# Performance work log

Hardware: AMD Instinct MI355X
Metric: run time of the kernel (lower is better)

Reference implementation:

```python
import jax, jax.numpy as jnp
import numpy as np

B, D_IN, M, D_MEM = 65536, 64, 2048, 64


def setup_inputs() -> dict:
    key = jax.random.key(0)
    k = jax.random.split(key, 5)
    glorot = lambda kk, shape: jax.random.uniform(
        kk, shape, jnp.float32,
        -jnp.sqrt(6.0 / (shape[0] + shape[1])), jnp.sqrt(6.0 / (shape[0] + shape[1])))
    return {
        "inputs": jax.random.normal(k[0], (B, D_IN), jnp.float32),
        "W_att": glorot(k[1], (D_IN, M)),
        "b_att": jnp.zeros((M,), jnp.float32),
        "W_write": glorot(k[2], (D_IN, D_MEM)),
        "b_write": jnp.zeros((D_MEM,), jnp.float32),
        "memory": glorot(k[3], (M, D_MEM)),
        "update_gate": jnp.full((M,), 0.5, jnp.float32),
    }


def reference(inputs, W_att, b_att, W_write, b_write, memory, update_gate):
    # Read attention: Dense(memory_size, softmax) -> [B, M]
    read_attention = jax.nn.softmax(inputs @ W_att + b_att, axis=-1)
    # Read: [B, M] @ [M, Dm] -> [B, Dm]
    read_vector = read_attention @ memory
    # Write candidate: Dense(memory_dim, tanh) -> [B, Dm]
    candidate_write = jnp.tanh(inputs @ W_write + b_write)
    aggregated_write = jnp.mean(candidate_write, axis=0)[None, :]  # [1, Dm]
    write_attention = jnp.mean(read_attention, axis=0)             # [M]
    update_weights = (write_attention * update_gate)[:, None]      # [M, 1]
    # Gated in-place memory update (returned as new state)
    new_memory = memory * (1.0 - update_weights) + update_weights * aggregated_write
    return read_vector, new_memory
```

## Files before the change

### kernel.cpp

```cpp
#include <hip/hip_runtime.h>
#include <hip/hip_bf16.h>

typedef unsigned int   u32;
typedef unsigned short u16;

typedef __bf16 bf16x8 __attribute__((ext_vector_type(8)));
typedef float  f32x4  __attribute__((ext_vector_type(4)));
typedef u32    u32x4  __attribute__((ext_vector_type(4)));
typedef u32    u32x2  __attribute__((ext_vector_type(2)));

union Frag { u32x4 u; bf16x8 b; };

#define MFMA16 __builtin_amdgcn_mfma_f32_16x16x32_bf16

#define B_ROWS 65536
#define D_IN   64
#define M_SZ   2048
#define D_MEM  64

#define WT_OFF      0
#define MEMT_OFF    262144
#define WWT_OFF     524288
#define CSF_OFF     532480
#define AGF_OFF     540672
#define CSP_OFF     540928
#define AGP_OFF     8929536
#define WS_REQUIRED 9191680

#define L2E 1.4426950408889634f

__device__ __forceinline__ float bf2f(u16 h) { return __uint_as_float(((u32)h) << 16); }
__device__ __forceinline__ u16 f2bf(float f) {
    u32 u = __float_as_uint(f);
    return (u16)((u + 0x7FFFu + ((u >> 16) & 1u)) >> 16);
}
#if defined(__has_builtin) && __has_builtin(__builtin_amdgcn_exp2f)
__device__ __forceinline__ float exp2fast(float x) { return __builtin_amdgcn_exp2f(x); }
#else
__device__ __forceinline__ float exp2fast(float x) { return __expf(x * 0.6931471805599453f); }
#endif
__device__ __forceinline__ float tanh_fast(float x) {
    const float e = exp2fast(x * (2.0f * L2E));
    return 1.0f - 2.0f * __builtin_amdgcn_rcpf(e + 1.0f);
}
__device__ __forceinline__ bool detect_bf16(const void* ug) {
    return ((const u32*)ug)[0] == 0x3F003F00u;
}
__device__ __forceinline__ float load_elem(const void* p, size_t i, bool isbf) {
    return isbf ? bf2f(((const u16*)p)[i]) : ((const float*)p)[i];
}

__device__ __forceinline__ u32 cvtpk_bf16(float lo, float hi) {
    u32 r;
    asm("v_cvt_pk_bf16_f32 %0, %1, %2" : "=v"(r) : "v"(lo), "v"(hi));
    return r;
}
#if defined(__has_builtin) && __has_builtin(__builtin_amdgcn_permlane32_swap) && \
    __has_builtin(__builtin_amdgcn_permlane16_swap)
__device__ __forceinline__ void pl32swap(u32& a, u32& b) {
    u32x2 r = __builtin_amdgcn_permlane32_swap(a, b, false, false);
    a = r[0]; b = r[1];
}
__device__ __forceinline__ void pl16swap(u32& a, u32& b) {
    u32x2 r = __builtin_amdgcn_permlane16_swap(a, b, false, false);
    a = r[0]; b = r[1];
}
#else
__device__ __forceinline__ void pl32swap(u32& a, u32& b) {
    asm("v_permlane32_swap_b32 %0, %1" : "+v"(a), "+v"(b));
}
__device__ __forceinline__ void pl16swap(u32& a, u32& b) {
    asm("v_permlane16_swap_b32 %0, %1" : "+v"(a), "+v"(b));
}
#endif
template<int CTRL>
__device__ __forceinline__ float xadd(float v) {
    int x = __builtin_amdgcn_update_dpp(0, __float_as_int(v), CTRL, 0xF, 0xF, true);
    return v + __int_as_float(x);
}

__global__ void __launch_bounds__(256)
prep_kernel(const void* Watt, const void* mem_in, const void* Wwr, const void* ug,
            u16* Wt, u16* memT, u16* Wwt, float* CSF)
{
    const bool isbf = detect_bf16(ug);
    const int b = blockIdx.x;
    const int t = threadIdx.x;
    if (b == 65) {
        for (int i = t; i < 2112; i += 256) CSF[i] = 0.f;
        return;
    }
    __shared__ u16 tile[64][65];
    const void* src; u16* dst; int R, C, rb, cb;
    if (b < 32)      { src = Watt;   dst = Wt;   R = 64;   C = 2048; rb = 0;           cb = b * 64; }
    else if (b < 64) { src = mem_in; dst = memT; R = 2048; C = 64;   rb = (b-32) * 64; cb = 0;      }
    else             { src = Wwr;    dst = Wwt;  R = 64;   C = 64;   rb = 0;           cb = 0;      }

#pragma unroll
    for (int j = 0; j < 16; ++j) {
        int e = j * 256 + t;
        int r = e >> 6, c = e & 63;
        float v = load_elem(src, (size_t)(rb + r) * C + cb + c, isbf);
        tile[r][c] = f2bf(v);
    }
    __syncthreads();
#pragma unroll
    for (int j = 0; j < 16; ++j) {
        int e = j * 256 + t;
        int c2 = e >> 6, r2 = e & 63;
        dst[(size_t)(cb + c2) * R + rb + r2] = tile[r2][c2];
    }
}

__global__ void __launch_bounds__(256, 2)
main_kernel(const void* x_in, const void* batt_in, const void* bwrite_in,
            const u16* __restrict__ Wt, const u16* __restrict__ memT,
            const u16* __restrict__ Wwt, const void* ug,
            float* CSF, float* AGF, u16* cs_part, u16* ag_part,
            int use_part, void* out)
{
    const bool isbf = detect_bf16(ug);
    const int tid = threadIdx.x;
    const int lane = tid & 63, wave = tid >> 6;
    const int quad = lane >> 4, l4 = lane & 15;
    const int rowbase = blockIdx.x * 128;
    const int wrow = blockIdx.x * 4 + wave;

    __shared__ __align__(16) u16 WtL[2][64][72];
    __shared__ __align__(16) u16 MeL[2][64][72];
    __shared__ __align__(16) float battL[2048];

    {
        const int i0 = tid * 8;
#pragma unroll
        for (int j = 0; j < 8; ++j)
            battL[i0 + j] = load_elem(batt_in, i0 + j, isbf) * L2E;
    }

    const int srow = tid >> 2, sg = (tid & 3) * 16;
    auto stageWt = [&](int c, int b) {
        const u16* g = Wt + ((size_t)c * 64 + srow) * 64 + sg;
        u32x4 v0 = *(const u32x4*)g;
        u32x4 v1 = *(const u32x4*)(g + 8);
        *(u32x4*)&WtL[b][srow][sg]     = v0;
        *(u32x4*)&WtL[b][srow][sg + 8] = v1;
    };
    auto stageMe = [&](int c, int b) {
        const u16* g = memT + (size_t)srow * 2048 + c * 64 + sg;
        u32x4 v0 = *(const u32x4*)g;
        u32x4 v1 = *(const u32x4*)(g + 8);
        *(u32x4*)&MeL[b][srow][sg]     = v0;
        *(u32x4*)&MeL[b][srow][sg + 8] = v1;
    };

    Frag a[2][2];
#pragma unroll
    for (int rg = 0; rg < 2; ++rg) {
        const int arow = rowbase + wave * 32 + rg * 16 + l4;
        if (isbf) {
            const u16* xp = (const u16*)x_in + (size_t)arow * 64 + quad * 8;
            a[rg][0].u = *(const u32x4*)xp;
            a[rg][1].u = *(const u32x4*)(xp + 32);
        } else {
            const float* xp = (const float*)x_in + (size_t)arow * 64 + quad * 8;
#pragma unroll
            for (int j = 0; j < 8; ++j) {
                ((u16*)&a[rg][0])[j] = f2bf(xp[j]);
                ((u16*)&a[rg][1])[j] = f2bf(xp[32 + j]);
            }
        }
    }
    const f32x4 zf = {0.f, 0.f, 0.f, 0.f};

    stageWt(0, 0);

    float agout = 0.f;
    {
        f32x4 accW[4][2];
#pragma unroll
        for (int t = 0; t < 4; ++t) {
            const u16* bp = Wwt + (size_t)(t * 16 + l4) * 64 + quad * 8;
            Frag b0, b1; b0.u = *(const u32x4*)bp; b1.u = *(const u32x4*)(bp + 32);
#pragma unroll
            for (int rg = 0; rg < 2; ++rg) {
                accW[t][rg] = MFMA16(a[rg][0].b, b0.b, zf, 0, 0, 0);
                accW[t][rg] = MFMA16(a[rg][1].b, b1.b, accW[t][rg], 0, 0, 0);
            }
        }
#pragma unroll
        for (int t = 0; t < 4; ++t) {
            const float bw = load_elem(bwrite_in, t * 16 + l4, isbf);
            float s = 0.f;
#pragma unroll
            for (int rg = 0; rg < 2; ++rg)
#pragma unroll
                for (int i = 0; i < 4; ++i) s += tanh_fast(accW[t][rg][i] + bw);
            s += __shfl_xor(s, 16, 64);
            s += __shfl_xor(s, 32, 64);
            if (quad == t) agout = s;
        }
    }
    if (use_part) ag_part[wrow * 64 + lane] = f2bf(agout);
    else          atomicAdd(&AGF[lane], agout);

    __syncthreads();

    float lsum[2] = {0.f, 0.f};
    for (int c = 0; c < 32; ++c) {
        const int buf = c & 1;
        if (c < 31) stageWt(c + 1, buf ^ 1);
        const int mbase = c * 64;
        Frag wb0[4], wb1[4]; f32x4 blv[4];
#pragma unroll
        for (int t = 0; t < 4; ++t) {
            wb0[t].u = *(const u32x4*)&WtL[buf][t * 16 + l4][quad * 8];
            wb1[t].u = *(const u32x4*)&WtL[buf][t * 16 + l4][32 + quad * 8];
            blv[t] = *(const f32x4*)&battL[mbase + t * 16 + quad * 4];
        }
#pragma unroll
        for (int t = 0; t < 4; ++t)
#pragma unroll
            for (int rg = 0; rg < 2; ++rg) {
                f32x4 acc = MFMA16(wb0[t].b, a[rg][0].b, zf, 0, 0, 0);
                acc = MFMA16(wb1[t].b, a[rg][1].b, acc, 0, 0, 0);
#pragma unroll
                for (int i = 0; i < 4; ++i)
                    lsum[rg] += exp2fast(fmaf(acc[i], L2E, blv[t][i]));
            }
        __syncthreads();
    }
    float invl[2];
#pragma unroll
    for (int rg = 0; rg < 2; ++rg) {
        float v = lsum[rg];
        v += __shfl_xor(v, 16, 64);
        v += __shfl_xor(v, 32, 64);
        invl[rg] = 1.f / v;
    }

    f32x4 oaccT[2][4] = {{zf,zf,zf,zf},{zf,zf,zf,zf}};
    stageWt(0, 0); stageMe(0, 0);
    __syncthreads();
    const bool sb0 = (l4 & 1), sb1 = (l4 & 2), sb2 = (l4 & 4), sb3 = (l4 & 8);
    for (int c = 0; c < 32; ++c) {
        const int buf = c & 1;
        if (c < 31) { stageWt(c + 1, buf ^ 1); stageMe(c + 1, buf ^ 1); }
        const int mbase = c * 64;
        Frag wb0[4], wb1[4], mb0[4], mb1[4]; f32x4 blv[4];
#pragma unroll
        for (int t = 0; t < 4; ++t) {
            wb0[t].u = *(const u32x4*)&WtL[buf][t * 16 + l4][quad * 8];
            wb1[t].u = *(const u32x4*)&WtL[buf][t * 16 + l4][32 + quad * 8];
            mb0[t].u = *(const u32x4*)&MeL[buf][t * 16 + l4][quad * 8];
            mb1[t].u = *(const u32x4*)&MeL[buf][t * 16 + l4][32 + quad * 8];
            blv[t] = *(const f32x4*)&battL[mbase + t * 16 + quad * 4];
        }
        u32 P0[2][4], P1[2][4];
        float c16[16];
#pragma unroll
        for (int j = 0; j < 16; ++j) c16[j] = 0.f;
#pragma unroll
        for (int t = 0; t < 4; ++t)
#pragma unroll
            for (int rg = 0; rg < 2; ++rg) {
                f32x4 acc = MFMA16(wb0[t].b, a[rg][0].b, zf, 0, 0, 0);
                acc = MFMA16(wb1[t].b, a[rg][1].b, acc, 0, 0, 0);
                const float p0 = exp2fast(fmaf(acc[0], L2E, blv[t][0])) * invl[rg];
                const float p1 = exp2fast(fmaf(acc[1], L2E, blv[t][1])) * invl[rg];
                const float p2 = exp2fast(fmaf(acc[2], L2E, blv[t][2])) * invl[rg];
                const float p3 = exp2fast(fmaf(acc[3], L2E, blv[t][3])) * invl[rg];
                c16[t * 4 + 0] += p0; c16[t * 4 + 1] += p1;
                c16[t * 4 + 2] += p2; c16[t * 4 + 3] += p3;
                P0[rg][t] = cvtpk_bf16(p0, p1);
                P1[rg][t] = cvtpk_bf16(p2, p3);
            }
#pragma unroll
        for (int rg = 0; rg < 2; ++rg)
#pragma unroll
            for (int cc = 0; cc < 2; ++cc) {
                u32 b0 = P0[rg][2 * cc], b2 = P0[rg][2 * cc + 1];
                u32 b1 = P1[rg][2 * cc], b3 = P1[rg][2 * cc + 1];
                pl32swap(b0, b2); pl16swap(b0, b2);
                pl32swap(b1, b3); pl16swap(b1, b3);
                Frag bf; bf.u = (u32x4){b0, b1, b2, b3};
#pragma unroll
                for (int dt = 0; dt < 4; ++dt) {
                    if (cc == 0)
                        oaccT[rg][dt] = MFMA16(mb0[dt].b, bf.b, oaccT[rg][dt], 0, 0, 0);
                    else
                        oaccT[rg][dt] = MFMA16(mb1[dt].b, bf.b, oaccT[rg][dt], 0, 0, 0);
                }
            }
        float u8[8];
#pragma unroll
        for (int k = 0; k < 8; ++k) {
            const float t0 = xadd<0xB1>(c16[2 * k]);
            const float t1 = xadd<0xB1>(c16[2 * k + 1]);
            u8[k] = sb0 ? t1 : t0;
        }
        float v4[4];
#pragma unroll
        for (int k = 0; k < 4; ++k) {
            const float t0 = xadd<0x4E>(u8[2 * k]);
            const float t1 = xadd<0x4E>(u8[2 * k + 1]);
            v4[k] = sb1 ? t1 : t0;
        }
        float w2[2];
#pragma unroll
        for (int k = 0; k < 2; ++k) {
            const float t0 = xadd<0x128>(v4[2 * k]);
            const float t1 = xadd<0x128>(v4[2 * k + 1]);
            w2[k] = sb3 ? t1 : t0;
        }
        const float f0 = w2[0] + __shfl_xor(w2[0], 4, 64);
        const float f1 = w2[1] + __shfl_xor(w2[1], 4, 64);
        const float csv = sb2 ? f1 : f0;
        const int tsel = ((l4 >> 3) & 1) | (((l4 >> 2) & 1) << 1);
        const int mout = mbase + tsel * 16 + quad * 4 + (l4 & 3);
        if (use_part) cs_part[(size_t)wrow * 2048 + mout] = f2bf(csv);
        else          atomicAdd(&CSF[mout], csv);
        __syncthreads();
    }

#pragma unroll
    for (int rg = 0; rg < 2; ++rg)
#pragma unroll
        for (int dt = 0; dt < 4; ++dt) {
            const int gr = rowbase + wave * 32 + rg * 16 + l4;
            const int d0 = dt * 16 + quad * 4;
            const f32x4 o = oaccT[rg][dt];
            if (isbf) {
                u32x2 w;
                w.x = cvtpk_bf16(o[0], o[1]);
                w.y = cvtpk_bf16(o[2], o[3]);
                *(u32x2*)&((u16*)out)[(size_t)gr * 64 + d0] = w;
            } else {
                *(f32x4*)&((float*)out)[(size_t)gr * 64 + d0] = o;
            }
        }
}

__global__ void __launch_bounds__(256)
reduce_kernel(const u16* __restrict__ cs_part, const u16* __restrict__ ag_part,
              float* CSF, float* AGF)
{
    const int b = blockIdx.x, t = threadIdx.x;
    if (b < 64) {
        const int m = (b & 7) * 256 + t;
        const int w0 = (b >> 3) * 256;
        float s = 0.f;
        for (int k = 0; k < 256; ++k) s += bf2f(cs_part[(size_t)(w0 + k) * 2048 + m]);
        atomicAdd(&CSF[m], s);
    } else if (t < 64) {
        const int w0 = (b - 64) * 512;
        float s = 0.f;
        for (int k = 0; k < 512; ++k) s += bf2f(ag_part[(w0 + k) * 64 + t]);
        atomicAdd(&AGF[t], s);
    }
}

__global__ void __launch_bounds__(256)
finalize_kernel(const void* mem_in, const void* ug,
                const float* __restrict__ CSF, const float* __restrict__ AGF,
                void* out)
{
    const bool isbf = detect_bf16(ug);
    const int idx = blockIdx.x * 256 + threadIdx.x;
    const int m = idx >> 6, d = idx & 63;
    const float wa  = CSF[m] * (1.f / 65536.f);
    const float agg = AGF[d] * (1.f / 65536.f);
    const float uw  = wa * load_elem(ug, m, isbf);
    const float mv  = load_elem(mem_in, idx, isbf);
    const float nm  = mv * (1.f - uw) + uw * agg;
    if (isbf) ((u16*)out)[(size_t)4194304 + idx] = f2bf(nm);
    else      ((float*)out)[(size_t)4194304 + idx] = nm;
}

extern "C" void kernel_launch(void* const* d_in, const int* in_sizes, int n_in,
                              void* d_out, int out_size, void* d_ws, size_t ws_size,
                              hipStream_t stream)
{
    (void)in_sizes; (void)n_in; (void)out_size;
    const void* x    = d_in[0];
    const void* Watt = d_in[1];
    const void* batt = d_in[2];
    const void* Wwr  = d_in[3];
    const void* bwr  = d_in[4];
    const void* mem  = d_in[5];
    const void* ug   = d_in[6];

    char* ws = (char*)d_ws;
    u16*   Wt      = (u16*)(ws + WT_OFF);
    u16*   memT    = (u16*)(ws + MEMT_OFF);
    u16*   Wwt     = (u16*)(ws + WWT_OFF);
    float* CSF     = (float*)(ws + CSF_OFF);
    float* AGF     = (float*)(ws + AGF_OFF);
    u16*   cs_part = (u16*)(ws + CSP_OFF);
    u16*   ag_part = (u16*)(ws + AGP_OFF);
    const int use_part = (ws_size >= (size_t)WS_REQUIRED) ? 1 : 0;

    prep_kernel<<<66, 256, 0, stream>>>(Watt, mem, Wwr, ug, Wt, memT, Wwt, CSF);
    main_kernel<<<512, 256, 0, stream>>>(x, batt, bwr, Wt, memT, Wwt, ug,
                                         CSF, AGF, cs_part, ag_part,
                                         use_part, d_out);
    if (use_part)
        reduce_kernel<<<68, 256, 0, stream>>>(cs_part, ag_part, CSF, AGF);
    finalize_kernel<<<512, 256, 0, stream>>>(mem, ug, CSF, AGF, d_out);
}
```

Baseline: 197.3 us.

## Stage 256-column chunks of attention weights and memory, reverse second pass

Replaces the double-buffered 64-column staging of W_att and memory with single-buffered 256-column chunks in LDS. This cuts the number of block-wide barriers per pass by a factor of four. The second pass walks chunks in reverse, so the last W_att chunk staged in the first pass is reused instead of reloaded. Softmax normalization of the probabilities fed to the read MFMA is deferred to a single scale on the output accumulators. In exchange, global loads no longer overlap compute within a block, LDS use roughly doubles (tight for two blocks per CU), and unnormalized exponentials are rounded to bf16.

```diff
diff --git a/kernel.cpp b/kernel.cpp
--- a/kernel.cpp
+++ b/kernel.cpp
@@ -126,8 +126,8 @@
     const int rowbase = blockIdx.x * 128;
     const int wrow = blockIdx.x * 4 + wave;
 
-    __shared__ __align__(16) u16 WtL[2][64][72];
-    __shared__ __align__(16) u16 MeL[2][64][72];
+    __shared__ __align__(16) u16 WtC[256][72];
+    __shared__ __align__(16) u16 MeC[64][264];
     __shared__ __align__(16) float battL[2048];
 
     {
@@ -137,20 +137,25 @@
             battL[i0 + j] = load_elem(batt_in, i0 + j, isbf) * L2E;
     }
 
-    const int srow = tid >> 2, sg = (tid & 3) * 16;
-    auto stageWt = [&](int c, int b) {
-        const u16* g = Wt + ((size_t)c * 64 + srow) * 64 + sg;
-        u32x4 v0 = *(const u32x4*)g;
-        u32x4 v1 = *(const u32x4*)(g + 8);
-        *(u32x4*)&WtL[b][srow][sg]     = v0;
-        *(u32x4*)&WtL[b][srow][sg + 8] = v1;
+    auto stageWtC = [&](int ch) {
+        const char* src = (const char*)(Wt + (size_t)ch * 16384);
+#pragma unroll
+        for (int j = 0; j < 8; ++j) {
+            const int o = j * 4096 + tid * 16;
+            const int m = o >> 7, k8 = (o & 127) >> 1;
+            u32x4 v = *(const u32x4*)(src + o);
+            *(u32x4*)&WtC[m][k8] = v;
+        }
     };
-    auto stageMe = [&](int c, int b) {
-        const u16* g = memT + (size_t)srow * 2048 + c * 64 + sg;
-        u32x4 v0 = *(const u32x4*)g;
-        u32x4 v1 = *(const u32x4*)(g + 8);
-        *(u32x4*)&MeL[b][srow][sg]     = v0;
-        *(u32x4*)&MeL[b][srow][sg + 8] = v1;
+    auto stageMeC = [&](int ch) {
+#pragma unroll
+        for (int j = 0; j < 8; ++j) {
+            const int d = j * 8 + (tid >> 5);
+            const int mo = (tid & 31) * 8;
+            const u16* g = memT + (size_t)d * 2048 + ch * 256 + mo;
+            u32x4 v = *(const u32x4*)g;
+            *(u32x4*)&MeC[d][mo] = v;
+        }
     };
 
     Frag a[2][2];
@@ -172,7 +177,7 @@
     }
     const f32x4 zf = {0.f, 0.f, 0.f, 0.f};
 
-    stageWt(0, 0);
+    stageWtC(0);
 
     float agout = 0.f;
     {
@@ -206,28 +211,30 @@
     __syncthreads();
 
     float lsum[2] = {0.f, 0.f};
-    for (int c = 0; c < 32; ++c) {
-        const int buf = c & 1;
-        if (c < 31) stageWt(c + 1, buf ^ 1);
-        const int mbase = c * 64;
-        Frag wb0[4], wb1[4]; f32x4 blv[4];
-#pragma unroll
-        for (int t = 0; t < 4; ++t) {
-            wb0[t].u = *(const u32x4*)&WtL[buf][t * 16 + l4][quad * 8];
-            wb1[t].u = *(const u32x4*)&WtL[buf][t * 16 + l4][32 + quad * 8];
-            blv[t] = *(const f32x4*)&battL[mbase + t * 16 + quad * 4];
-        }
-#pragma unroll
-        for (int t = 0; t < 4; ++t)
-#pragma unroll
-            for (int rg = 0; rg < 2; ++rg) {
-                f32x4 acc = MFMA16(wb0[t].b, a[rg][0].b, zf, 0, 0, 0);
-                acc = MFMA16(wb1[t].b, a[rg][1].b, acc, 0, 0, 0);
-#pragma unroll
-                for (int i = 0; i < 4; ++i)
-                    lsum[rg] += exp2fast(fmaf(acc[i], L2E, blv[t][i]));
-            }
+    for (int ch = 0; ch < 8; ++ch) {
+        for (int cc = 0; cc < 4; ++cc) {
+            const int mb = cc * 64;
+            const int mbase = ch * 256 + mb;
+            Frag wb0[4], wb1[4]; f32x4 blv[4];
+#pragma unroll
+            for (int t = 0; t < 4; ++t) {
+                wb0[t].u = *(const u32x4*)&WtC[mb + t * 16 + l4][quad * 8];
+                wb1[t].u = *(const u32x4*)&WtC[mb + t * 16 + l4][32 + quad * 8];
+                blv[t] = *(const f32x4*)&battL[mbase + t * 16 + quad * 4];
+            }
+#pragma unroll
+            for (int t = 0; t < 4; ++t)
+#pragma unroll
+                for (int rg = 0; rg < 2; ++rg) {
+                    f32x4 acc = MFMA16(wb0[t].b, a[rg][0].b, zf, 0, 0, 0);
+                    acc = MFMA16(wb1[t].b, a[rg][1].b, acc, 0, 0, 0);
+#pragma unroll
+                    for (int i = 0; i < 4; ++i)
+                        lsum[rg] += exp2fast(fmaf(acc[i], L2E, blv[t][i]));
+                }
+        }
         __syncthreads();
+        if (ch < 7) { stageWtC(ch + 1); __syncthreads(); }
     }
     float invl[2];
 #pragma unroll
@@ -239,87 +246,92 @@
     }
 
     f32x4 oaccT[2][4] = {{zf,zf,zf,zf},{zf,zf,zf,zf}};
-    stageWt(0, 0); stageMe(0, 0);
+    stageMeC(7);
     __syncthreads();
     const bool sb0 = (l4 & 1), sb1 = (l4 & 2), sb2 = (l4 & 4), sb3 = (l4 & 8);
-    for (int c = 0; c < 32; ++c) {
-        const int buf = c & 1;
-        if (c < 31) { stageWt(c + 1, buf ^ 1); stageMe(c + 1, buf ^ 1); }
-        const int mbase = c * 64;
-        Frag wb0[4], wb1[4], mb0[4], mb1[4]; f32x4 blv[4];
-#pragma unroll
-        for (int t = 0; t < 4; ++t) {
-            wb0[t].u = *(const u32x4*)&WtL[buf][t * 16 + l4][quad * 8];
-            wb1[t].u = *(const u32x4*)&WtL[buf][t * 16 + l4][32 + quad * 8];
-            mb0[t].u = *(const u32x4*)&MeL[buf][t * 16 + l4][quad * 8];
-            mb1[t].u = *(const u32x4*)&MeL[buf][t * 16 + l4][32 + quad * 8];
-            blv[t] = *(const f32x4*)&battL[mbase + t * 16 + quad * 4];
-        }
-        u32 P0[2][4], P1[2][4];
-        float c16[16];
-#pragma unroll
-        for (int j = 0; j < 16; ++j) c16[j] = 0.f;
-#pragma unroll
-        for (int t = 0; t < 4; ++t)
-#pragma unroll
-            for (int rg = 0; rg < 2; ++rg) {
-                f32x4 acc = MFMA16(wb0[t].b, a[rg][0].b, zf, 0, 0, 0);
-                acc = MFMA16(wb1[t].b, a[rg][1].b, acc, 0, 0, 0);
-                const float p0 = exp2fast(fmaf(acc[0], L2E, blv[t][0])) * invl[rg];
-                const float p1 = exp2fast(fmaf(acc[1], L2E, blv[t][1])) * invl[rg];
-                const float p2 = exp2fast(fmaf(acc[2], L2E, blv[t][2])) * invl[rg];
-                const float p3 = exp2fast(fmaf(acc[3], L2E, blv[t][3])) * invl[rg];
-                c16[t * 4 + 0] += p0; c16[t * 4 + 1] += p1;
-                c16[t * 4 + 2] += p2; c16[t * 4 + 3] += p3;
-                P0[rg][t] = cvtpk_bf16(p0, p1);
-                P1[rg][t] = cvtpk_bf16(p2, p3);
-            }
-#pragma unroll
-        for (int rg = 0; rg < 2; ++rg)
-#pragma unroll
-            for (int cc = 0; cc < 2; ++cc) {
-                u32 b0 = P0[rg][2 * cc], b2 = P0[rg][2 * cc + 1];
-                u32 b1 = P1[rg][2 * cc], b3 = P1[rg][2 * cc + 1];
-                pl32swap(b0, b2); pl16swap(b0, b2);
-                pl32swap(b1, b3); pl16swap(b1, b3);
-                Frag bf; bf.u = (u32x4){b0, b1, b2, b3};
-#pragma unroll
-                for (int dt = 0; dt < 4; ++dt) {
-                    if (cc == 0)
-                        oaccT[rg][dt] = MFMA16(mb0[dt].b, bf.b, oaccT[rg][dt], 0, 0, 0);
-                    else
-                        oaccT[rg][dt] = MFMA16(mb1[dt].b, bf.b, oaccT[rg][dt], 0, 0, 0);
+    for (int ch = 7; ch >= 0; --ch) {
+        for (int cc = 0; cc < 4; ++cc) {
+            const int mb = cc * 64;
+            const int mbase = ch * 256 + mb;
+            Frag wb0[4], wb1[4], mb0[4], mb1[4]; f32x4 blv[4];
+#pragma unroll
+            for (int t = 0; t < 4; ++t) {
+                wb0[t].u = *(const u32x4*)&WtC[mb + t * 16 + l4][quad * 8];
+                wb1[t].u = *(const u32x4*)&WtC[mb + t * 16 + l4][32 + quad * 8];
+                mb0[t].u = *(const u32x4*)&MeC[t * 16 + l4][mb + quad * 8];
+                mb1[t].u = *(const u32x4*)&MeC[t * 16 + l4][mb + 32 + quad * 8];
+                blv[t] = *(const f32x4*)&battL[mbase + t * 16 + quad * 4];
+            }
+            u32 P0[2][4], P1[2][4];
+            float c16[16];
+#pragma unroll
+            for (int j = 0; j < 16; ++j) c16[j] = 0.f;
+#pragma unroll
+            for (int t = 0; t < 4; ++t)
+#pragma unroll
+                for (int rg = 0; rg < 2; ++rg) {
+                    f32x4 acc = MFMA16(wb0[t].b, a[rg][0].b, zf, 0, 0, 0);
+                    acc = MFMA16(wb1[t].b, a[rg][1].b, acc, 0, 0, 0);
+                    const float il = invl[rg];
+                    const float e0 = exp2fast(fmaf(acc[0], L2E, blv[t][0]));
+                    const float e1 = exp2fast(fmaf(acc[1], L2E, blv[t][1]));
+                    const float e2 = exp2fast(fmaf(acc[2], L2E, blv[t][2]));
+                    const float e3 = exp2fast(fmaf(acc[3], L2E, blv[t][3]));
+                    c16[t * 4 + 0] = fmaf(e0, il, c16[t * 4 + 0]);
+                    c16[t * 4 + 1] = fmaf(e1, il, c16[t * 4 + 1]);
+                    c16[t * 4 + 2] = fmaf(e2, il, c16[t * 4 + 2]);
+                    c16[t * 4 + 3] = fmaf(e3, il, c16[t * 4 + 3]);
+                    P0[rg][t] = cvtpk_bf16(e0, e1);
+                    P1[rg][t] = cvtpk_bf16(e2, e3);
                 }
-            }
-        float u8[8];
-#pragma unroll
-        for (int k = 0; k < 8; ++k) {
-            const float t0 = xadd<0xB1>(c16[2 * k]);
-            const float t1 = xadd<0xB1>(c16[2 * k + 1]);
-            u8[k] = sb0 ? t1 : t0;
-        }
-        float v4[4];
-#pragma unroll
-        for (int k = 0; k < 4; ++k) {
-            const float t0 = xadd<0x4E>(u8[2 * k]);
-            const float t1 = xadd<0x4E>(u8[2 * k + 1]);
-            v4[k] = sb1 ? t1 : t0;
-        }
-        float w2[2];
-#pragma unroll
-        for (int k = 0; k < 2; ++k) {
-            const float t0 = xadd<0x128>(v4[2 * k]);
-            const float t1 = xadd<0x128>(v4[2 * k + 1]);
-            w2[k] = sb3 ? t1 : t0;
-        }
-        const float f0 = w2[0] + __shfl_xor(w2[0], 4, 64);
-        const float f1 = w2[1] + __shfl_xor(w2[1], 4, 64);
-        const float csv = sb2 ? f1 : f0;
-        const int tsel = ((l4 >> 3) & 1) | (((l4 >> 2) & 1) << 1);
-        const int mout = mbase + tsel * 16 + quad * 4 + (l4 & 3);
-        if (use_part) cs_part[(size_t)wrow * 2048 + mout] = f2bf(csv);
-        else          atomicAdd(&CSF[mout], csv);
+#pragma unroll
+            for (int rg = 0; rg < 2; ++rg)
+#pragma unroll
+                for (int cc2 = 0; cc2 < 2; ++cc2) {
+                    u32 b0 = P0[rg][2 * cc2], b2 = P0[rg][2 * cc2 + 1];
+                    u32 b1 = P1[rg][2 * cc2], b3 = P1[rg][2 * cc2 + 1];
+                    pl32swap(b0, b2); pl16swap(b0, b2);
+                    pl32swap(b1, b3); pl16swap(b1, b3);
+                    Frag bf; bf.u = (u32x4){b0, b1, b2, b3};
+#pragma unroll
+                    for (int dt = 0; dt < 4; ++dt) {
+                        if (cc2 == 0)
+                            oaccT[rg][dt] = MFMA16(mb0[dt].b, bf.b, oaccT[rg][dt], 0, 0, 0);
+                        else
+                            oaccT[rg][dt] = MFMA16(mb1[dt].b, bf.b, oaccT[rg][dt], 0, 0, 0);
+                    }
+                }
+            float u8[8];
+#pragma unroll
+            for (int k = 0; k < 8; ++k) {
+                const float t0 = xadd<0xB1>(c16[2 * k]);
+                const float t1 = xadd<0xB1>(c16[2 * k + 1]);
+                u8[k] = sb0 ? t1 : t0;
+            }
+            float v4[4];
+#pragma unroll
+            for (int k = 0; k < 4; ++k) {
+                const float t0 = xadd<0x4E>(u8[2 * k]);
+                const float t1 = xadd<0x4E>(u8[2 * k + 1]);
+                v4[k] = sb1 ? t1 : t0;
+            }
+            float w2[2];
+#pragma unroll
+            for (int k = 0; k < 2; ++k) {
+                const float t0 = xadd<0x128>(v4[2 * k]);
+                const float t1 = xadd<0x128>(v4[2 * k + 1]);
+                w2[k] = sb3 ? t1 : t0;
+            }
+            const float f0 = w2[0] + __shfl_xor(w2[0], 4, 64);
+            const float f1 = w2[1] + __shfl_xor(w2[1], 4, 64);
+            const float csv = sb2 ? f1 : f0;
+            const int tsel = ((l4 >> 3) & 1) | (((l4 >> 2) & 1) << 1);
+            const int mout = mbase + tsel * 16 + quad * 4 + (l4 & 3);
+            if (use_part) cs_part[(size_t)wrow * 2048 + mout] = f2bf(csv);
+            else          atomicAdd(&CSF[mout], csv);
+        }
         __syncthreads();
+        if (ch > 0) { stageWtC(ch - 1); stageMeC(ch - 1); __syncthreads(); }
     }
 
 #pragma unroll
@@ -328,7 +340,7 @@
         for (int dt = 0; dt < 4; ++dt) {
             const int gr = rowbase + wave * 32 + rg * 16 + l4;
             const int d0 = dt * 16 + quad * 4;
-            const f32x4 o = oaccT[rg][dt];
+            const f32x4 o = oaccT[rg][dt] * invl[rg];
             if (isbf) {
                 u32x2 w;
                 w.x = cvtpk_bf16(o[0], o[1]);
```

Measured after the change: 196.3 us. About the same (-0.5%).
